# Performance work log

Measured on AMD Instinct MI355X. Metric: run time of the kernel, lower is better.

## Reference

```python
import jax, jax.numpy as jnp
import numpy as np

N_NODES = 50000
N_EDGES = 800000
HIDDEN = 64
DEPTH = 3
NUM_GRAPHS = 256
NUM_CLASSES = 1
BN_EPS = 1e-5


def setup_inputs() -> dict:
    key = jax.random.key(0)
    ks = jax.random.split(key, 12)
    x = jax.random.normal(ks[0], (N_NODES, HIDDEN), dtype=jnp.float32)
    edge_index = jax.random.randint(ks[1], (2, N_EDGES), 0, N_NODES, dtype=jnp.int32)
    batch = jnp.sort(jax.random.randint(ks[2], (N_NODES,), 0, NUM_GRAPHS, dtype=jnp.int32))
    s = 1.0 / np.sqrt(HIDDEN)
    W1 = jax.random.uniform(ks[3], (DEPTH, HIDDEN, HIDDEN), jnp.float32, -s, s)
    b1 = jax.random.uniform(ks[4], (DEPTH, HIDDEN), jnp.float32, -s, s)
    W2 = jax.random.uniform(ks[5], (DEPTH, HIDDEN, HIDDEN), jnp.float32, -s, s)
    b2 = jax.random.uniform(ks[6], (DEPTH, HIDDEN), jnp.float32, -s, s)
    gamma = jnp.ones((DEPTH, HIDDEN), jnp.float32)
    beta = jnp.zeros((DEPTH, HIDDEN), jnp.float32)
    Wf = jax.random.uniform(ks[7], (HIDDEN, NUM_CLASSES), jnp.float32, -s, s)
    bf = jax.random.uniform(ks[8], (NUM_CLASSES,), jnp.float32, -s, s)
    return {"x": x, "edge_index": edge_index, "batch": batch,
            "W1": W1, "b1": b1, "W2": W2, "b2": b2,
            "gamma": gamma, "beta": beta, "Wf": Wf, "bf": bf}


def reference(x, edge_index, batch, W1, b1, W2, b2, gamma, beta, Wf, bf):
    src, dst = edge_index[0], edge_index[1]
    for i in range(DEPTH):
        # GINConv: (1+eps)*x + scatter-add of neighbor features (eps=0)
        agg = jnp.zeros_like(x).at[dst].add(x[src])
        h = x + agg
        h = jax.nn.relu(h @ W1[i] + b1[i])
        h = jax.nn.relu(h @ W2[i] + b2[i])
        # BatchNorm over node dimension (training-mode batch stats)
        mean = h.mean(axis=0)
        var = ((h - mean) ** 2).mean(axis=0)
        h = (h - mean) * jax.lax.rsqrt(var + BN_EPS) * gamma[i] + beta[i]
        x = jax.nn.relu(h)
    pooled = jax.ops.segment_sum(x, batch, num_segments=NUM_GRAPHS)  # [G, H]
    return pooled @ Wf + bf
```

## Files before the change

### kernel.cpp

```cpp
#include <hip/hip_runtime.h>

#define HIDDEN_C 64
#define NCHUNK 256

typedef __attribute__((ext_vector_type(8))) short bf16x8;
typedef __attribute__((ext_vector_type(8))) unsigned short u16x8;
typedef __attribute__((ext_vector_type(4))) float f32x4;

__device__ __forceinline__ float4 f4zero() { return make_float4(0.f, 0.f, 0.f, 0.f); }

__device__ __forceinline__ unsigned short f2bf(float f) {
    unsigned u = __float_as_uint(f);
    u += 0x7FFF + ((u >> 16) & 1);
    return (unsigned short)(u >> 16);
}
__device__ __forceinline__ float bf2f(unsigned short h) {
    return __uint_as_float(((unsigned)h) << 16);
}

__device__ __forceinline__ int swz_idx(int row, int k) {
    return row * 64 + ((((k >> 3) ^ (row & 7)) << 3) | (k & 7));
}

__global__ __launch_bounds__(256) void k_blocksum(const int* __restrict__ deg,
                                                  int* __restrict__ partial, int n) {
    int base = blockIdx.x * 1024 + threadIdx.x * 4;
    int s = 0;
#pragma unroll
    for (int k = 0; k < 4; ++k) {
        int i = base + k;
        if (i < n) s += deg[i];
    }
    __shared__ int red[256];
    red[threadIdx.x] = s;
    __syncthreads();
    for (int d = 128; d > 0; d >>= 1) {
        if (threadIdx.x < d) red[threadIdx.x] += red[threadIdx.x + d];
        __syncthreads();
    }
    if (threadIdx.x == 0) partial[blockIdx.x] = red[0];
}

__global__ __launch_bounds__(256) void k_scanpartial(int* __restrict__ partial,
                                                     int* __restrict__ last_slot,
                                                     int nBlocks, int nE) {
    __shared__ int buf[256];
    int tid = threadIdx.x;
    int v = (tid < nBlocks) ? partial[tid] : 0;
    buf[tid] = v;
    __syncthreads();
    for (int d = 1; d < 256; d <<= 1) {
        int t = (tid >= d) ? buf[tid - d] : 0;
        __syncthreads();
        buf[tid] += t;
        __syncthreads();
    }
    if (tid < nBlocks) partial[tid] = buf[tid] - v;
    if (tid == 0) last_slot[0] = nE;
}

__global__ __launch_bounds__(256) void k_writeptr(const int* __restrict__ deg,
                                                  const int* __restrict__ partial,
                                                  int* __restrict__ outp, int n) {
    int tid = threadIdx.x;
    int base = blockIdx.x * 1024 + tid * 4;
    int d[4];
    int s = 0;
#pragma unroll
    for (int k = 0; k < 4; ++k) {
        int i = base + k;
        d[k] = (i < n) ? deg[i] : 0;
        s += d[k];
    }
    __shared__ int buf[256];
    buf[tid] = s;
    __syncthreads();
    for (int dd = 1; dd < 256; dd <<= 1) {
        int t = (tid >= dd) ? buf[tid - dd] : 0;
        __syncthreads();
        buf[tid] += t;
        __syncthreads();
    }
    int off = partial[blockIdx.x] + buf[tid] - s;
#pragma unroll
    for (int k = 0; k < 4; ++k) {
        int i = base + k;
        if (i < n) {
            outp[i] = off;
            off += d[k];
        }
    }
}

__global__ __launch_bounds__(256) void k_bcount(const int* __restrict__ dst,
                                                int* __restrict__ cnt,
                                                float* __restrict__ statsZ,
                                                int nE, int chunkSz, int nBuckets) {
    __shared__ int h[1024];
    int c = blockIdx.x, tid = threadIdx.x;
    if (c == 0) {
        for (int i = tid; i < 384; i += 256) statsZ[i] = 0.f;
    }
    for (int i = tid; i < nBuckets; i += 256) h[i] = 0;
    __syncthreads();
    int beg = c * chunkSz;
    int end = beg + chunkSz; if (end > nE) end = nE;
    int e = beg + tid;
    for (; e + 256 < end; e += 512) {
        int d0 = dst[e];
        int d1 = dst[e + 256];
        atomicAdd(&h[d0 >> 6], 1);
        atomicAdd(&h[d1 >> 6], 1);
    }
    if (e < end) atomicAdd(&h[dst[e] >> 6], 1);
    __syncthreads();
    for (int i = tid; i < nBuckets; i += 256) cnt[i * NCHUNK + c] = h[i];
}

__global__ __launch_bounds__(256) void k_bscatter(const int* __restrict__ src,
                                                  const int* __restrict__ dst,
                                                  const int* __restrict__ eoff,
                                                  unsigned* __restrict__ ebuf,
                                                  int nE, int chunkSz, int nBuckets) {
    __shared__ int cur[1024];
    int c = blockIdx.x, tid = threadIdx.x;
    for (int i = tid; i < nBuckets; i += 256) cur[i] = eoff[i * NCHUNK + c];
    __syncthreads();
    int beg = c * chunkSz;
    int end = beg + chunkSz; if (end > nE) end = nE;
    int e = beg + tid;
    for (; e + 256 < end; e += 512) {
        int d0 = dst[e];
        int d1 = dst[e + 256];
        int s0 = src[e];
        int s1 = src[e + 256];
        int p0 = atomicAdd(&cur[d0 >> 6], 1);
        int p1 = atomicAdd(&cur[d1 >> 6], 1);
        ebuf[p0] = ((unsigned)(d0 & 63) << 16) | (unsigned)s0;
        ebuf[p1] = ((unsigned)(d1 & 63) << 16) | (unsigned)s1;
    }
    if (e < end) {
        int d = dst[e];
        int pos = atomicAdd(&cur[d >> 6], 1);
        ebuf[pos] = ((unsigned)(d & 63) << 16) | (unsigned)src[e];
    }
}

__global__ __launch_bounds__(256) void k_bfill(const unsigned* __restrict__ ebuf,
                                               const int* __restrict__ eoff,
                                               int* __restrict__ rowptr,
                                               int* __restrict__ col,
                                               int nNodes, int nE, int nBuckets) {
    __shared__ int deg[64], cur[64];
    int b = blockIdx.x, tid = threadIdx.x;
    int lo = eoff[b * NCHUNK];
    int hi = (b + 1 < nBuckets) ? eoff[(b + 1) * NCHUNK] : nE;
    if (tid < 64) deg[tid] = 0;
    __syncthreads();
    for (int e = lo + tid; e < hi; e += 256) atomicAdd(&deg[ebuf[e] >> 16], 1);
    __syncthreads();
    if (tid < 64) {
        int d = deg[tid];
        int s = d;
        for (int o = 1; o < 64; o <<= 1) {
            int t = __shfl_up(s, o, 64);
            if (tid >= o) s += t;
        }
        int st = s - d;
        cur[tid] = lo + st;
        int node = b * 64 + tid;
        if (node < nNodes) rowptr[node] = lo + st;
    }
    __syncthreads();
    for (int e = lo + tid; e < hi; e += 256) {
        unsigned pk = ebuf[e];
        int pos = atomicAdd(&cur[pk >> 16], 1);
        col[pos] = (int)(pk & 0xFFFFu);
    }
}

__global__ __launch_bounds__(256) void k_wprep(const float* __restrict__ W1,
                                               const float* __restrict__ W2,
                                               unsigned short* __restrict__ wt) {
    __shared__ unsigned short s[8192];
    int b = blockIdx.x;
    int layer = b >> 1;
    const float* src = ((b & 1) ? W2 : W1) + (size_t)layer * 4096;
    int tid = threadIdx.x;
    int k = tid >> 2;
    int f0 = (tid & 3) * 16;
    const float* srcp = src + k * 64 + f0;
#pragma unroll
    for (int j4 = 0; j4 < 4; ++j4) {
        float4 wv = *(const float4*)(srcp + j4 * 4);
        float c[4] = {wv.x, wv.y, wv.z, wv.w};
        int f = f0 + j4 * 4;
#pragma unroll
        for (int j = 0; j < 4; ++j) {
            unsigned short h = f2bf(c[j]);
            int ix = swz_idx(f + j, k);
            s[ix] = h;
            s[4096 + ix] = f2bf(c[j] - bf2f(h));
        }
    }
    __syncthreads();
    uint4* dst = (uint4*)(wt + (size_t)b * 8192);
    const uint4* sp = (const uint4*)s;
#pragma unroll
    for (int it = 0; it < 4; ++it) dst[it * 256 + tid] = sp[it * 256 + tid];
}

template <bool DOBN>
__global__ __launch_bounds__(256) void k_aggbn(const float4* __restrict__ x4,
                                               const int* __restrict__ rowptr,
                                               const int* __restrict__ col,
                                               const float* __restrict__ stats,
                                               const float* __restrict__ gamma,
                                               const float* __restrict__ beta,
                                               float4* __restrict__ h4,
                                               int nNodes, float invN) {
    int wid = threadIdx.x >> 6;
    int lane = threadIdx.x & 63;
    int grp = lane >> 4;
    int l16 = lane & 15;
    int n = blockIdx.x * 4 + wid;
    if (n >= nNodes) return;

    float4 sc = make_float4(1.f, 1.f, 1.f, 1.f);
    float4 sh = f4zero();
    if (DOBN) {
        float4 s  = ((const float4*)stats)[l16];
        float4 q  = ((const float4*)stats)[16 + l16];
        float4 ga = ((const float4*)gamma)[l16];
        float4 be = ((const float4*)beta)[l16];
        float m;
        m = s.x * invN; sc.x = ga.x * rsqrtf(q.x * invN - m * m + 1e-5f); sh.x = be.x - m * sc.x;
        m = s.y * invN; sc.y = ga.y * rsqrtf(q.y * invN - m * m + 1e-5f); sh.y = be.y - m * sc.y;
        m = s.z * invN; sc.z = ga.z * rsqrtf(q.z * invN - m * m + 1e-5f); sh.z = be.z - m * sc.z;
        m = s.w * invN; sc.w = ga.w * rsqrtf(q.w * invN - m * m + 1e-5f); sh.w = be.w - m * sc.w;
    }

    float4 acc = f4zero();
    {
        float4 v = x4[(size_t)n * 16 + l16];
        if (DOBN) {
            v.x = fmaxf(fmaf(v.x, sc.x, sh.x), 0.f);
            v.y = fmaxf(fmaf(v.y, sc.y, sh.y), 0.f);
            v.z = fmaxf(fmaf(v.z, sc.z, sh.z), 0.f);
            v.w = fmaxf(fmaf(v.w, sc.w, sh.w), 0.f);
        }
        if (grp == 0) acc = v;
    }

    int lo = rowptr[n], hi = rowptr[n + 1];
    int e = lo;
    for (; e + 8 <= hi; e += 8) {
        int i0 = col[e + grp];
        int i1 = col[e + 4 + grp];
        float4 v0 = x4[(size_t)i0 * 16 + l16];
        float4 v1 = x4[(size_t)i1 * 16 + l16];
        if (DOBN) {
            v0.x = fmaxf(fmaf(v0.x, sc.x, sh.x), 0.f);
            v0.y = fmaxf(fmaf(v0.y, sc.y, sh.y), 0.f);
            v0.z = fmaxf(fmaf(v0.z, sc.z, sh.z), 0.f);
            v0.w = fmaxf(fmaf(v0.w, sc.w, sh.w), 0.f);
            v1.x = fmaxf(fmaf(v1.x, sc.x, sh.x), 0.f);
            v1.y = fmaxf(fmaf(v1.y, sc.y, sh.y), 0.f);
            v1.z = fmaxf(fmaf(v1.z, sc.z, sh.z), 0.f);
            v1.w = fmaxf(fmaf(v1.w, sc.w, sh.w), 0.f);
        }
        acc.x += v0.x + v1.x; acc.y += v0.y + v1.y;
        acc.z += v0.z + v1.z; acc.w += v0.w + v1.w;
    }
    for (; e < hi; e += 4) {
        int ee = e + grp;
        bool ok = ee < hi;
        int idx = col[ok ? ee : (hi - 1)];
        float4 v = x4[(size_t)idx * 16 + l16];
        if (DOBN) {
            v.x = fmaxf(fmaf(v.x, sc.x, sh.x), 0.f);
            v.y = fmaxf(fmaf(v.y, sc.y, sh.y), 0.f);
            v.z = fmaxf(fmaf(v.z, sc.z, sh.z), 0.f);
            v.w = fmaxf(fmaf(v.w, sc.w, sh.w), 0.f);
        }
        if (ok) {
            acc.x += v.x; acc.y += v.y; acc.z += v.z; acc.w += v.w;
        }
    }

    acc.x += __shfl_xor(acc.x, 16, 64); acc.y += __shfl_xor(acc.y, 16, 64);
    acc.z += __shfl_xor(acc.z, 16, 64); acc.w += __shfl_xor(acc.w, 16, 64);
    acc.x += __shfl_xor(acc.x, 32, 64); acc.y += __shfl_xor(acc.y, 32, 64);
    acc.z += __shfl_xor(acc.z, 32, 64); acc.w += __shfl_xor(acc.w, 32, 64);

    if (lane < 16) h4[(size_t)n * 16 + l16] = acc;
}

__global__ __launch_bounds__(256, 5) void k_mlp(const float* __restrict__ h_in,
                                                float* __restrict__ h_out,
                                                const unsigned short* __restrict__ wt1,
                                                const float* __restrict__ b1,
                                                const unsigned short* __restrict__ wt2,
                                                const float* __restrict__ b2,
                                                float* __restrict__ stats,
                                                int nNodes) {
    __shared__ __align__(16) unsigned short smem16[16384];
    unsigned short* sA_hi = smem16;
    unsigned short* sA_lo = smem16 + 4096;
    unsigned short* sW_hi = smem16 + 8192;
    unsigned short* sW_lo = smem16 + 12288;

    int tid = threadIdx.x;
    int n0 = blockIdx.x * 64;
    int lane = tid & 63;
    int w = tid >> 6;
    int lr = lane & 15;
    int q = lane >> 4;
    int r0 = w * 16;

#pragma unroll
    for (int it = 0; it < 2; ++it) {
        int idx = it * 256 + tid;
        int row = idx >> 3, ch = idx & 7;
        float4 v0 = f4zero(), v1 = f4zero();
        if (n0 + row < nNodes) {
            const float4* p = (const float4*)(h_in + (size_t)(n0 + row) * 64 + ch * 8);
            v0 = p[0]; v1 = p[1];
        }
        float f[8] = {v0.x, v0.y, v0.z, v0.w, v1.x, v1.y, v1.z, v1.w};
        u16x8 hv, lv;
#pragma unroll
        for (int j = 0; j < 8; ++j) {
            unsigned short h = f2bf(f[j]);
            hv[j] = h;
            lv[j] = f2bf(f[j] - bf2f(h));
        }
        int off = row * 64 + ((ch ^ (row & 7)) << 3);
        *(u16x8*)(sA_hi + off) = hv;
        *(u16x8*)(sA_lo + off) = lv;
    }
    {
        uint4* d = (uint4*)sW_hi;
        const uint4* s = (const uint4*)wt1;
#pragma unroll
        for (int it = 0; it < 4; ++it) d[it * 256 + tid] = s[it * 256 + tid];
    }
    __syncthreads();

    f32x4 acc[4];

#define GEMM_SPLIT(AHI, ALO, BIAS)                                               \
    {                                                                            \
        int rowA = r0 + lr;                                                      \
        const unsigned short* pah = AHI + rowA * 64;                             \
        const unsigned short* pal = ALO + rowA * 64;                             \
        int sr = rowA & 7;                                                       \
        bf16x8 ah0 = *(const bf16x8*)(pah + ((q ^ sr) << 3));                    \
        bf16x8 ah1 = *(const bf16x8*)(pah + (((4 + q) ^ sr) << 3));              \
        bf16x8 al0 = *(const bf16x8*)(pal + ((q ^ sr) << 3));                    \
        bf16x8 al1 = *(const bf16x8*)(pal + (((4 + q) ^ sr) << 3));              \
        _Pragma("unroll")                                                        \
        for (int ct = 0; ct < 4; ++ct) {                                         \
            int f = ct * 16 + lr;                                                \
            const unsigned short* pbh = sW_hi + f * 64;                          \
            const unsigned short* pbl = sW_lo + f * 64;                          \
            int sf = f & 7;                                                      \
            bf16x8 bh0 = *(const bf16x8*)(pbh + ((q ^ sf) << 3));                \
            bf16x8 bh1 = *(const bf16x8*)(pbh + (((4 + q) ^ sf) << 3));          \
            bf16x8 bl0 = *(const bf16x8*)(pbl + ((q ^ sf) << 3));                \
            bf16x8 bl1 = *(const bf16x8*)(pbl + (((4 + q) ^ sf) << 3));          \
            float bias = BIAS[f];                                                \
            f32x4 c = {bias, bias, bias, bias};                                  \
            c = __builtin_amdgcn_mfma_f32_16x16x32_bf16(al0, bh0, c, 0, 0, 0);   \
            c = __builtin_amdgcn_mfma_f32_16x16x32_bf16(al1, bh1, c, 0, 0, 0);   \
            c = __builtin_amdgcn_mfma_f32_16x16x32_bf16(ah0, bl0, c, 0, 0, 0);   \
            c = __builtin_amdgcn_mfma_f32_16x16x32_bf16(ah1, bl1, c, 0, 0, 0);   \
            c = __builtin_amdgcn_mfma_f32_16x16x32_bf16(ah0, bh0, c, 0, 0, 0);   \
            c = __builtin_amdgcn_mfma_f32_16x16x32_bf16(ah1, bh1, c, 0, 0, 0);   \
            acc[ct] = c;                                                         \
        }                                                                        \
    }

    GEMM_SPLIT(sA_hi, sA_lo, b1)

    __syncthreads();

#pragma unroll
    for (int ct = 0; ct < 4; ++ct) {
        int f = ct * 16 + lr;
#pragma unroll
        for (int rg = 0; rg < 4; ++rg) {
            int row = r0 + q * 4 + rg;
            float v = fmaxf(acc[ct][rg], 0.f);
            unsigned short h = f2bf(v);
            int ix = swz_idx(row, f);
            sA_hi[ix] = h;
            sA_lo[ix] = f2bf(v - bf2f(h));
        }
    }
    {
        uint4* d = (uint4*)sW_hi;
        const uint4* s = (const uint4*)wt2;
#pragma unroll
        for (int it = 0; it < 4; ++it) d[it * 256 + tid] = s[it * 256 + tid];
    }
    __syncthreads();

    GEMM_SPLIT(sA_hi, sA_lo, b2)

    __syncthreads();
#undef GEMM_SPLIT

    float* sS = (float*)sW_hi;
    float* sQ = sS + 256;

#pragma unroll
    for (int ct = 0; ct < 4; ++ct) {
        int f = ct * 16 + lr;
        float sp = 0.f, qp = 0.f;
#pragma unroll
        for (int rg = 0; rg < 4; ++rg) {
            int row = r0 + q * 4 + rg;
            float v = fmaxf(acc[ct][rg], 0.f);
            if (n0 + row < nNodes) {
                h_out[(size_t)(n0 + row) * 64 + f] = v;
                sp += v;
                qp += v * v;
            }
        }
        sp += __shfl_xor(sp, 16, 64); qp += __shfl_xor(qp, 16, 64);
        sp += __shfl_xor(sp, 32, 64); qp += __shfl_xor(qp, 32, 64);
        if (q == 0) {
            sS[w * 64 + f] = sp;
            sQ[w * 64 + f] = qp;
        }
    }
    __syncthreads();
    if (tid < 64) {
        float S = sS[tid] + sS[64 + tid] + sS[128 + tid] + sS[192 + tid];
        atomicAdd(&stats[tid], S);
    } else if (tid < 128) {
        int f = tid - 64;
        float Q = sQ[f] + sQ[64 + f] + sQ[128 + f] + sQ[192 + f];
        atomicAdd(&stats[64 + f], Q);
    }
}

__device__ __forceinline__ int lower_bound_dev(const int* a, int n, int key) {
    int lo = 0, hi = n;
    while (lo < hi) {
        int mid = (lo + hi) >> 1;
        if (a[mid] < key) lo = mid + 1; else hi = mid;
    }
    return lo;
}

__global__ __launch_bounds__(256) void k_pool(const float4* __restrict__ x4,
                                              const int* __restrict__ batch,
                                              const float* __restrict__ stats,
                                              const float* __restrict__ gamma,
                                              const float* __restrict__ beta,
                                              const float* __restrict__ Wf,
                                              const float* __restrict__ bf,
                                              float* __restrict__ out,
                                              int nNodes, float invN) {
    int wid = threadIdx.x >> 6;
    int lane = threadIdx.x & 63;
    int grp = lane >> 4;
    int l16 = lane & 15;
    int g = blockIdx.x * 4 + wid;

    float4 sc, sh;
    {
        float4 s  = ((const float4*)stats)[l16];
        float4 q  = ((const float4*)stats)[16 + l16];
        float4 ga = ((const float4*)gamma)[l16];
        float4 be = ((const float4*)beta)[l16];
        float m;
        m = s.x * invN; sc.x = ga.x * rsqrtf(q.x * invN - m * m + 1e-5f); sh.x = be.x - m * sc.x;
        m = s.y * invN; sc.y = ga.y * rsqrtf(q.y * invN - m * m + 1e-5f); sh.y = be.y - m * sc.y;
        m = s.z * invN; sc.z = ga.z * rsqrtf(q.z * invN - m * m + 1e-5f); sh.z = be.z - m * sc.z;
        m = s.w * invN; sc.w = ga.w * rsqrtf(q.w * invN - m * m + 1e-5f); sh.w = be.w - m * sc.w;
    }

    int lo = lower_bound_dev(batch, nNodes, g);
    int hi = lower_bound_dev(batch, nNodes, g + 1);

    float4 acc = f4zero();
    for (int r = lo + grp; r < hi; r += 4) {
        float4 v = x4[(size_t)r * 16 + l16];
        acc.x += fmaxf(fmaf(v.x, sc.x, sh.x), 0.f);
        acc.y += fmaxf(fmaf(v.y, sc.y, sh.y), 0.f);
        acc.z += fmaxf(fmaf(v.z, sc.z, sh.z), 0.f);
        acc.w += fmaxf(fmaf(v.w, sc.w, sh.w), 0.f);
    }
    acc.x += __shfl_xor(acc.x, 16, 64); acc.y += __shfl_xor(acc.y, 16, 64);
    acc.z += __shfl_xor(acc.z, 16, 64); acc.w += __shfl_xor(acc.w, 16, 64);
    acc.x += __shfl_xor(acc.x, 32, 64); acc.y += __shfl_xor(acc.y, 32, 64);
    acc.z += __shfl_xor(acc.z, 32, 64); acc.w += __shfl_xor(acc.w, 32, 64);

    float4 wf = ((const float4*)Wf)[l16];
    float p = acc.x * wf.x + acc.y * wf.y + acc.z * wf.z + acc.w * wf.w;
    p += __shfl_xor(p, 1, 64);
    p += __shfl_xor(p, 2, 64);
    p += __shfl_xor(p, 4, 64);
    p += __shfl_xor(p, 8, 64);
    if (lane == 0) out[g] = p + bf[0];
}

extern "C" void kernel_launch(void* const* d_in, const int* in_sizes, int n_in,
                              void* d_out, int out_size, void* d_ws, size_t ws_size,
                              hipStream_t stream) {
    const float* x_in  = (const float*)d_in[0];
    const int*   ei    = (const int*)d_in[1];
    const int*   batch = (const int*)d_in[2];
    const float* W1    = (const float*)d_in[3];
    const float* b1    = (const float*)d_in[4];
    const float* W2    = (const float*)d_in[5];
    const float* b2    = (const float*)d_in[6];
    const float* gamma = (const float*)d_in[7];
    const float* beta  = (const float*)d_in[8];
    const float* Wf    = (const float*)d_in[9];
    const float* bf    = (const float*)d_in[10];

    const int nNodes = in_sizes[0] / HIDDEN_C;
    const int nE = in_sizes[1] / 2;
    const int* src = ei;
    const int* dst = ei + nE;

    const int nBuckets = (nNodes + 63) / 64;
    const int nTot = nBuckets * NCHUNK;
    const int chunkSz = (nE + NCHUNK - 1) / NCHUNK;
    const int scanBlocks = (nTot + 1023) / 1024;
    const float invN = 1.f / (float)nNodes;

    const size_t NB = (size_t)nNodes * HIDDEN_C * sizeof(float);
    char* ws = (char*)d_ws;
    float*    bufA    = (float*)ws;
    float*    bufB    = (float*)(ws + NB);
    float*    stats   = (float*)(ws + 2 * NB);
    unsigned short* wtbuf = (unsigned short*)(ws + 2 * NB + 4096);
    int*      rowptr  = (int*)(ws + 2 * NB + 4096 + 98304);
    int*      partial = rowptr + nNodes + 64;
    int*      col     = partial + 256;
    unsigned* ebuf    = (unsigned*)bufB;
    int*      cnt     = (int*)((char*)bufB + (size_t)nE * 4);
    int*      eoff    = cnt + nTot + 64;

    const int mlpGrid = nBuckets;
    const int aggGrid = (nNodes + 3) / 4;

    k_wprep<<<6, 256, 0, stream>>>(W1, W2, wtbuf);
    k_bcount<<<NCHUNK, 256, 0, stream>>>(dst, cnt, stats, nE, chunkSz, nBuckets);
    k_blocksum<<<scanBlocks, 256, 0, stream>>>(cnt, partial, nTot);
    k_scanpartial<<<1, 256, 0, stream>>>(partial, rowptr + nNodes, scanBlocks, nE);
    k_writeptr<<<scanBlocks, 256, 0, stream>>>(cnt, partial, eoff, nTot);
    k_bscatter<<<NCHUNK, 256, 0, stream>>>(src, dst, eoff, ebuf, nE, chunkSz, nBuckets);
    k_bfill<<<nBuckets, 256, 0, stream>>>(ebuf, eoff, rowptr, col, nNodes, nE, nBuckets);

    const float* prev_h = x_in;
    float* cur = bufA;
    for (int i = 0; i < 3; ++i) {
        if (i == 0) {
            k_aggbn<false><<<aggGrid, 256, 0, stream>>>((const float4*)prev_h, rowptr, col,
                                                        nullptr, nullptr, nullptr,
                                                        (float4*)cur, nNodes, invN);
        } else {
            k_aggbn<true><<<aggGrid, 256, 0, stream>>>((const float4*)prev_h, rowptr, col,
                                                       stats + (size_t)(i - 1) * 128,
                                                       gamma + (size_t)(i - 1) * 64,
                                                       beta + (size_t)(i - 1) * 64,
                                                       (float4*)cur, nNodes, invN);
        }
        k_mlp<<<mlpGrid, 256, 0, stream>>>(cur, cur,
                                           wtbuf + (size_t)(2 * i) * 8192, b1 + (size_t)i * 64,
                                           wtbuf + (size_t)(2 * i + 1) * 8192, b2 + (size_t)i * 64,
                                           stats + (size_t)i * 128, nNodes);
        prev_h = cur;
        cur = (cur == bufA) ? bufB : bufA;
    }

    k_pool<<<64, 256, 0, stream>>>((const float4*)prev_h, batch,
                                   stats + 256, gamma + 128, beta + 128,
                                   Wf, bf, (float*)d_out, nNodes, invN);
}
```

Before: 244.4 us.

## Halve MLP tile rows, split output columns across waves, prefetch W2, widen bucket kernels

The MLP kernel now handles 32 nodes per block instead of 64. Each wave computes a 16-row by 32-column output quadrant, which doubles the grid and cuts shared memory per block. The second weight matrix is prefetched into registers at kernel start, so its global load overlaps the first GEMM. The bucket count and scatter kernels move to 512 threads per block to speed edge processing. In exchange, per-block weight staging in LDS is repeated across twice as many blocks, and register pressure rises from the W2 prefetch.

```diff
diff --git a/kernel.cpp b/kernel.cpp
--- a/kernel.cpp
+++ b/kernel.cpp
@@ -92,48 +92,48 @@
     }
 }
 
-__global__ __launch_bounds__(256) void k_bcount(const int* __restrict__ dst,
+__global__ __launch_bounds__(512) void k_bcount(const int* __restrict__ dst,
                                                 int* __restrict__ cnt,
                                                 float* __restrict__ statsZ,
                                                 int nE, int chunkSz, int nBuckets) {
     __shared__ int h[1024];
     int c = blockIdx.x, tid = threadIdx.x;
     if (c == 0) {
-        for (int i = tid; i < 384; i += 256) statsZ[i] = 0.f;
-    }
-    for (int i = tid; i < nBuckets; i += 256) h[i] = 0;
+        for (int i = tid; i < 384; i += 512) statsZ[i] = 0.f;
+    }
+    for (int i = tid; i < nBuckets; i += 512) h[i] = 0;
     __syncthreads();
     int beg = c * chunkSz;
     int end = beg + chunkSz; if (end > nE) end = nE;
     int e = beg + tid;
-    for (; e + 256 < end; e += 512) {
+    for (; e + 512 < end; e += 1024) {
         int d0 = dst[e];
-        int d1 = dst[e + 256];
+        int d1 = dst[e + 512];
         atomicAdd(&h[d0 >> 6], 1);
         atomicAdd(&h[d1 >> 6], 1);
     }
     if (e < end) atomicAdd(&h[dst[e] >> 6], 1);
     __syncthreads();
-    for (int i = tid; i < nBuckets; i += 256) cnt[i * NCHUNK + c] = h[i];
-}
-
-__global__ __launch_bounds__(256) void k_bscatter(const int* __restrict__ src,
+    for (int i = tid; i < nBuckets; i += 512) cnt[i * NCHUNK + c] = h[i];
+}
+
+__global__ __launch_bounds__(512) void k_bscatter(const int* __restrict__ src,
                                                   const int* __restrict__ dst,
                                                   const int* __restrict__ eoff,
                                                   unsigned* __restrict__ ebuf,
                                                   int nE, int chunkSz, int nBuckets) {
     __shared__ int cur[1024];
     int c = blockIdx.x, tid = threadIdx.x;
-    for (int i = tid; i < nBuckets; i += 256) cur[i] = eoff[i * NCHUNK + c];
+    for (int i = tid; i < nBuckets; i += 512) cur[i] = eoff[i * NCHUNK + c];
     __syncthreads();
     int beg = c * chunkSz;
     int end = beg + chunkSz; if (end > nE) end = nE;
     int e = beg + tid;
-    for (; e + 256 < end; e += 512) {
+    for (; e + 512 < end; e += 1024) {
         int d0 = dst[e];
-        int d1 = dst[e + 256];
+        int d1 = dst[e + 512];
         int s0 = src[e];
-        int s1 = src[e + 256];
+        int s1 = src[e + 512];
         int p0 = atomicAdd(&cur[d0 >> 6], 1);
         int p1 = atomicAdd(&cur[d1 >> 6], 1);
         ebuf[p0] = ((unsigned)(d0 & 63) << 16) | (unsigned)s0;
@@ -304,24 +304,27 @@
                                                 const float* __restrict__ b2,
                                                 float* __restrict__ stats,
                                                 int nNodes) {
-    __shared__ __align__(16) unsigned short smem16[16384];
+    __shared__ __align__(16) unsigned short smem16[12288];
     unsigned short* sA_hi = smem16;
-    unsigned short* sA_lo = smem16 + 4096;
-    unsigned short* sW_hi = smem16 + 8192;
-    unsigned short* sW_lo = smem16 + 12288;
+    unsigned short* sA_lo = smem16 + 2048;
+    unsigned short* sW_hi = smem16 + 4096;
+    unsigned short* sW_lo = smem16 + 8192;
 
     int tid = threadIdx.x;
-    int n0 = blockIdx.x * 64;
+    int n0 = blockIdx.x * 32;
     int lane = tid & 63;
     int w = tid >> 6;
     int lr = lane & 15;
     int q = lane >> 4;
-    int r0 = w * 16;
-
-#pragma unroll
-    for (int it = 0; it < 2; ++it) {
-        int idx = it * 256 + tid;
-        int row = idx >> 3, ch = idx & 7;
+    int rt = w >> 1;
+    int c0 = (w & 1) * 2;
+
+    uint4 w2r[4];
+#pragma unroll
+    for (int it = 0; it < 4; ++it) w2r[it] = ((const uint4*)wt2)[it * 256 + tid];
+
+    {
+        int row = tid >> 3, ch = tid & 7;
         float4 v0 = f4zero(), v1 = f4zero();
         if (n0 + row < nNodes) {
             const float4* p = (const float4*)(h_in + (size_t)(n0 + row) * 64 + ch * 8);
@@ -347,21 +350,21 @@
     }
     __syncthreads();
 
-    f32x4 acc[4];
-
-#define GEMM_SPLIT(AHI, ALO, BIAS)                                               \
+    f32x4 acc[2];
+
+#define GEMM_SPLIT(BIAS)                                                         \
     {                                                                            \
-        int rowA = r0 + lr;                                                      \
-        const unsigned short* pah = AHI + rowA * 64;                             \
-        const unsigned short* pal = ALO + rowA * 64;                             \
+        int rowA = rt * 16 + lr;                                                 \
+        const unsigned short* pah = sA_hi + rowA * 64;                           \
+        const unsigned short* pal = sA_lo + rowA * 64;                           \
         int sr = rowA & 7;                                                       \
         bf16x8 ah0 = *(const bf16x8*)(pah + ((q ^ sr) << 3));                    \
         bf16x8 ah1 = *(const bf16x8*)(pah + (((4 + q) ^ sr) << 3));              \
         bf16x8 al0 = *(const bf16x8*)(pal + ((q ^ sr) << 3));                    \
         bf16x8 al1 = *(const bf16x8*)(pal + (((4 + q) ^ sr) << 3));              \
         _Pragma("unroll")                                                        \
-        for (int ct = 0; ct < 4; ++ct) {                                         \
-            int f = ct * 16 + lr;                                                \
+        for (int t = 0; t < 2; ++t) {                                            \
+            int f = (c0 + t) * 16 + lr;                                          \
             const unsigned short* pbh = sW_hi + f * 64;                          \
             const unsigned short* pbl = sW_lo + f * 64;                          \
             int sf = f & 7;                                                      \
@@ -377,21 +380,21 @@
             c = __builtin_amdgcn_mfma_f32_16x16x32_bf16(ah1, bl1, c, 0, 0, 0);   \
             c = __builtin_amdgcn_mfma_f32_16x16x32_bf16(ah0, bh0, c, 0, 0, 0);   \
             c = __builtin_amdgcn_mfma_f32_16x16x32_bf16(ah1, bh1, c, 0, 0, 0);   \
-            acc[ct] = c;                                                         \
+            acc[t] = c;                                                          \
         }                                                                        \
     }
 
-    GEMM_SPLIT(sA_hi, sA_lo, b1)
-
-    __syncthreads();
-
-#pragma unroll
-    for (int ct = 0; ct < 4; ++ct) {
-        int f = ct * 16 + lr;
+    GEMM_SPLIT(b1)
+
+    __syncthreads();
+
+#pragma unroll
+    for (int t = 0; t < 2; ++t) {
+        int f = (c0 + t) * 16 + lr;
 #pragma unroll
         for (int rg = 0; rg < 4; ++rg) {
-            int row = r0 + q * 4 + rg;
-            float v = fmaxf(acc[ct][rg], 0.f);
+            int row = rt * 16 + q * 4 + rg;
+            float v = fmaxf(acc[t][rg], 0.f);
             unsigned short h = f2bf(v);
             int ix = swz_idx(row, f);
             sA_hi[ix] = h;
@@ -400,28 +403,27 @@
     }
     {
         uint4* d = (uint4*)sW_hi;
-        const uint4* s = (const uint4*)wt2;
-#pragma unroll
-        for (int it = 0; it < 4; ++it) d[it * 256 + tid] = s[it * 256 + tid];
-    }
-    __syncthreads();
-
-    GEMM_SPLIT(sA_hi, sA_lo, b2)
+#pragma unroll
+        for (int it = 0; it < 4; ++it) d[it * 256 + tid] = w2r[it];
+    }
+    __syncthreads();
+
+    GEMM_SPLIT(b2)
 
     __syncthreads();
 #undef GEMM_SPLIT
 
     float* sS = (float*)sW_hi;
-    float* sQ = sS + 256;
-
-#pragma unroll
-    for (int ct = 0; ct < 4; ++ct) {
-        int f = ct * 16 + lr;
+    float* sQ = sS + 128;
+
+#pragma unroll
+    for (int t = 0; t < 2; ++t) {
+        int f = (c0 + t) * 16 + lr;
         float sp = 0.f, qp = 0.f;
 #pragma unroll
         for (int rg = 0; rg < 4; ++rg) {
-            int row = r0 + q * 4 + rg;
-            float v = fmaxf(acc[ct][rg], 0.f);
+            int row = rt * 16 + q * 4 + rg;
+            float v = fmaxf(acc[t][rg], 0.f);
             if (n0 + row < nNodes) {
                 h_out[(size_t)(n0 + row) * 64 + f] = v;
                 sp += v;
@@ -431,18 +433,16 @@
         sp += __shfl_xor(sp, 16, 64); qp += __shfl_xor(qp, 16, 64);
         sp += __shfl_xor(sp, 32, 64); qp += __shfl_xor(qp, 32, 64);
         if (q == 0) {
-            sS[w * 64 + f] = sp;
-            sQ[w * 64 + f] = qp;
+            sS[rt * 64 + f] = sp;
+            sQ[rt * 64 + f] = qp;
         }
     }
     __syncthreads();
     if (tid < 64) {
-        float S = sS[tid] + sS[64 + tid] + sS[128 + tid] + sS[192 + tid];
-        atomicAdd(&stats[tid], S);
+        atomicAdd(&stats[tid], sS[tid] + sS[64 + tid]);
     } else if (tid < 128) {
         int f = tid - 64;
-        float Q = sQ[f] + sQ[64 + f] + sQ[128 + f] + sQ[192 + f];
-        atomicAdd(&stats[64 + f], Q);
+        atomicAdd(&stats[64 + f], sQ[f] + sQ[64 + f]);
     }
 }
 
@@ -547,15 +547,15 @@
     int*      cnt     = (int*)((char*)bufB + (size_t)nE * 4);
     int*      eoff    = cnt + nTot + 64;
 
-    const int mlpGrid = nBuckets;
+    const int mlpGrid = (nNodes + 31) / 32;
     const int aggGrid = (nNodes + 3) / 4;
 
     k_wprep<<<6, 256, 0, stream>>>(W1, W2, wtbuf);
-    k_bcount<<<NCHUNK, 256, 0, stream>>>(dst, cnt, stats, nE, chunkSz, nBuckets);
+    k_bcount<<<NCHUNK, 512, 0, stream>>>(dst, cnt, stats, nE, chunkSz, nBuckets);
     k_blocksum<<<scanBlocks, 256, 0, stream>>>(cnt, partial, nTot);
     k_scanpartial<<<1, 256, 0, stream>>>(partial, rowptr + nNodes, scanBlocks, nE);
     k_writeptr<<<scanBlocks, 256, 0, stream>>>(cnt, partial, eoff, nTot);
-    k_bscatter<<<NCHUNK, 256, 0, stream>>>(src, dst, eoff, ebuf, nE, chunkSz, nBuckets);
+    k_bscatter<<<NCHUNK, 512, 0, stream>>>(src, dst, eoff, ebuf, nE, chunkSz, nBuckets);
     k_bfill<<<nBuckets, 256, 0, stream>>>(ebuf, eoff, rowptr, col, nNodes, nE, nBuckets);
 
     const float* prev_h = x_in;
```

Measured after the change: 298.7 us. +22.2%, slower.
